# Performance work log

Hardware: AMD Instinct MI355X
Metric: run time of the kernel (lower is better)

## Reference

```python
import jax, jax.numpy as jnp
import numpy as np

N_TP = 4  # number of heterogeneous agent types (experts)


def _mlp(x, w1, b1, w2, b2, w3, b3):
    h = jax.nn.relu(x @ w1 + b1)
    h = jax.nn.relu(h @ w2 + b2)
    return h @ w3 + b3


def setup_inputs() -> dict:
    key = jax.random.key(0)
    ks = jax.random.split(key, 12)
    T, A, D, H, NA = 2048, 128, 64, 64, 16
    s = 0.05
    return {
        "obs": jax.random.normal(ks[0], (T, A, D), dtype=jnp.float32),
        "hete_pick": jax.random.randint(ks[1], (T, A), 0, N_TP, dtype=jnp.int64),
        "gp_sel_summary": jax.random.uniform(ks[2], (T, N_TP), dtype=jnp.float32),
        "W1": jax.random.normal(ks[3], (N_TP, D + N_TP, H), dtype=jnp.float32) * s,
        "b1": jnp.zeros((N_TP, H), jnp.float32),
        "W2": jax.random.normal(ks[4], (N_TP, H, H), dtype=jnp.float32) * s,
        "b2": jnp.zeros((N_TP, H), jnp.float32),
        "W3": jax.random.normal(ks[5], (N_TP, H, NA), dtype=jnp.float32) * s,
        "b3": jnp.zeros((N_TP, NA), jnp.float32),
        "cW1": jax.random.normal(ks[6], (D + N_TP, H), dtype=jnp.float32) * s,
        "cb1": jnp.zeros((H,), jnp.float32),
        "cW2": jax.random.normal(ks[7], (H, H), dtype=jnp.float32) * s,
        "cb2": jnp.zeros((H,), jnp.float32),
        "cW3": jax.random.normal(ks[8], (H, 1), dtype=jnp.float32) * s,
        "cb3": jnp.zeros((1,), jnp.float32),
    }


def reference(obs, hete_pick, gp_sel_summary, W1, b1, W2, b2, W3, b3,
              cW1, cb1, cW2, cb2, cW3, cb3):
    T, A, D = obs.shape
    n_tp = W1.shape[0]
    # hete_info_obs: broadcast group-selection summary over agents, concat to obs
    hete_info = jnp.broadcast_to(gp_sel_summary[:, None, :], (T, A, n_tp))
    x = jnp.concatenate([obs, hete_info.astype(obs.dtype)], axis=-1)  # [T,A,D+n_tp]
    xf = x.reshape(T * A, D + n_tp)
    tp = hete_pick.reshape(T * A)
    # per-type dispatch: mask -> sub-net -> scatter back (expressed as masked select)
    logits = jnp.zeros((T * A, W3.shape[-1]), obs.dtype)
    for t in range(n_tp):
        out_t = _mlp(xf, W1[t], b1[t], W2[t], b2[t], W3[t], b3[t])
        logits = jnp.where((tp == t)[:, None], out_t, logits)
    # central critic runs on all agents
    value = _mlp(xf, cW1, cb1, cW2, cb2, cW3, cb3)  # [T*A,1]
    out = jnp.concatenate([logits, value], axis=-1)  # [T*A, n_action+1]
    return out.reshape(T, A, -1)
```

## Files before the change

### kernel.cpp

```cpp
#include <hip/hip_runtime.h>
#include <stdint.h>


typedef float v4f __attribute__((ext_vector_type(4)));
typedef short v8s __attribute__((ext_vector_type(8)));
typedef short v4s __attribute__((ext_vector_type(4)));
typedef float v4fa __attribute__((ext_vector_type(4), aligned(4)));

#define HS_STR 136
#define WP2_OFF 30720
#define WP3_OFF 51200

#define SEL4(te, a0, a1, a2, a3) \
    ((te) < 2 ? ((te) == 0 ? (a0) : (a1)) : ((te) == 2 ? (a2) : (a3)))

static __device__ __forceinline__ short f2bf(float f) {
    union { __bf16 b; short s; } u;
    u.b = (__bf16)f;
    return u.s;
}

static __device__ __forceinline__ v4s pack4_relu(const v4f a, const v4fa bias) {
    v4s r;
    r[0] = f2bf(fmaxf(a[0] + bias[0], 0.f));
    r[1] = f2bf(fmaxf(a[1] + bias[1], 0.f));
    r[2] = f2bf(fmaxf(a[2] + bias[2], 0.f));
    r[3] = f2bf(fmaxf(a[3] + bias[3], 0.f));
    return r;
}

__global__ void prep_kernel(const float* __restrict__ W1, const float* __restrict__ cW1,
                            const float* __restrict__ W2, const float* __restrict__ cW2,
                            const float* __restrict__ W3, const float* __restrict__ cW3,
                            short* __restrict__ wp) {
    int b = blockIdx.x, lane = threadIdx.x;
    int nl = lane & 15, quad = lane >> 4;
    short frag[8];
    if (b < 60) {
        int e = b / 12, rem = b % 12, ks = rem / 4, nt = rem % 4;
        int n = nt * 16 + nl;
#pragma unroll
        for (int j = 0; j < 8; j++) {
            int k = ks * 32 + quad * 8 + j;
            float v = 0.f;
            if (k < 68) v = (e < 4) ? W1[(e * 68 + k) * 64 + n] : cW1[k * 64 + n];
            frag[j] = f2bf(v);
        }
    } else if (b < 100) {
        int u = b - 60, e = u / 8, ks = (u % 8) / 4, nt = u % 4;
        int n = nt * 16 + nl;
#pragma unroll
        for (int j = 0; j < 8; j++) {
            int k = ks * 32 + quad * 8 + j;
            frag[j] = f2bf((e < 4) ? W2[(e * 64 + k) * 64 + n] : cW2[k * 64 + n]);
        }
    } else {
        int u = b - 100;
#pragma unroll
        for (int j = 0; j < 8; j++) {
            int ks = (u < 8) ? (u & 1) : (u - 8);
            int k  = ks * 32 + quad * 8 + j;
            float v;
            if (u < 8) { int ee = u >> 1; v = W3[(ee * 64 + k) * 16 + nl]; }
            else       { v = (nl == 0) ? cW3[k] : 0.f; }
            frag[j] = f2bf(v);
        }
    }
    v8s pk = { frag[0], frag[1], frag[2], frag[3], frag[4], frag[5], frag[6], frag[7] };
    *(v8s*)(wp + (size_t)b * 512 + lane * 8) = pk;
}


__global__ __launch_bounds__(256, 4) void main_kernel(
    const float* __restrict__ obs, const int* __restrict__ hete,
    const float* __restrict__ gp, const short* __restrict__ wp,
    const float* __restrict__ b1, const float* __restrict__ b2, const float* __restrict__ b3,
    const float* __restrict__ cb1, const float* __restrict__ cb2, const float* __restrict__ cb3,
    float* __restrict__ out)
{
    __shared__ __align__(16) short buf[128 * HS_STR];
    __shared__ int rowtok[128];
    __shared__ int tslot[128];
    __shared__ int wcnt[2][4];

    short* xs = buf;
    short* hs = buf;

    const int b = blockIdx.x;
    const int tid = threadIdx.x, lane = tid & 63, w = tid >> 6;
    const int ml = lane & 15, quad = lane >> 4;
    const size_t base = (size_t)b * 128;

    const int ltk = tid >> 1, hh = tid & 1;
    const float4* src = (const float4*)(obs + (base + ltk) * 64 + hh * 32);
    float4 f[8];
#pragma unroll
    for (int t = 0; t < 8; t++) f[t] = src[t];

    const float* gpb = gp + (size_t)b * 4;
    float g0 = gpb[0], g1 = gpb[1], g2 = gpb[2], g3 = gpb[3];

    int e = 0, rank = 0;
    if (tid < 128) {
        e = hete[base + tid];
        unsigned long long ltm = (1ull << lane) - 1ull;
        unsigned long long m0 = __ballot(e == 0);
        unsigned long long m1 = __ballot(e == 1);
        unsigned long long m2 = __ballot(e == 2);
        unsigned long long m3 = __ballot(e == 3);
        if      (e == 0) rank = __popcll(m0 & ltm);
        else if (e == 1) rank = __popcll(m1 & ltm);
        else if (e == 2) rank = __popcll(m2 & ltm);
        else             rank = __popcll(m3 & ltm);
        if (lane == 0) {
            wcnt[w][0] = __popcll(m0); wcnt[w][1] = __popcll(m1);
            wcnt[w][2] = __popcll(m2); wcnt[w][3] = __popcll(m3);
        }
    }
    __syncthreads();

    const int c0 = wcnt[0][0] + wcnt[1][0];
    const int c1 = wcnt[0][1] + wcnt[1][1];
    const int c2 = wcnt[0][2] + wcnt[1][2];
    const int gs1 = c0, gs2 = c0 + c1, gs3 = c0 + c1 + c2;

    if (tid < 128) {
        int gsE  = SEL4(e, 0, gs1, gs2, gs3);
        int woff = (w == 1) ? wcnt[0][e] : 0;
        int slot = gsE + woff + rank;
        rowtok[slot] = tid;
        tslot[tid]   = slot;
    }
    __syncthreads();

    int teA[8];
#pragma unroll
    for (int mt = 0; mt < 8; mt++)
        teA[mt] = (mt * 16 >= gs1) + (mt * 16 >= gs2) + (mt * 16 >= gs3);

    {
        int s  = tslot[ltk];
        int rb = s * HS_STR + hh * 32;
#pragma unroll
        for (int t = 0; t < 4; t++) {
            float4 a0 = f[2 * t], a1 = f[2 * t + 1];
            v8s pk = { f2bf(a0.x), f2bf(a0.y), f2bf(a0.z), f2bf(a0.w),
                       f2bf(a1.x), f2bf(a1.y), f2bf(a1.z), f2bf(a1.w) };
            *(v8s*)&xs[rb + t * 8] = pk;
        }
        if (hh) {
            v8s pg = { f2bf(g0), f2bf(g1), f2bf(g2), f2bf(g3), 0, 0, 0, 0 };
            v8s z8 = { 0, 0, 0, 0, 0, 0, 0, 0 };
            *(v8s*)&xs[s * HS_STR + 64] = pg;
            *(v8s*)&xs[s * HS_STR + 72] = z8;
            *(v8s*)&xs[s * HS_STR + 80] = z8;
            *(v8s*)&xs[s * HS_STR + 88] = z8;
        }
    }
    __syncthreads();

    v4f accE[8], accC[8];
#pragma unroll
    for (int mt = 0; mt < 8; mt++) { accE[mt] = (v4f){0,0,0,0}; accC[mt] = (v4f){0,0,0,0}; }

    v8s cf1[3];
#pragma unroll
    for (int ks = 0; ks < 3; ks++)
        cf1[ks] = *(const v8s*)(wp + (size_t)((12 + ks) * 4 + w) * 512 + lane * 8);

#pragma unroll
    for (int ks = 0; ks < 3; ks++) {
#pragma unroll
        for (int mt = 0; mt < 8; mt++) {
            v8s aW = *(const v8s*)(wp + (size_t)((teA[mt] * 3 + ks) * 4 + w) * 512 + lane * 8);
            v8s xB = *(const v8s*)&xs[(mt * 16 + ml) * HS_STR + ks * 32 + quad * 8];
            accE[mt] = __builtin_amdgcn_mfma_f32_16x16x32_bf16(aW, xB, accE[mt], 0, 0, 0);
            accC[mt] = __builtin_amdgcn_mfma_f32_16x16x32_bf16(cf1[ks], xB, accC[mt], 0, 0, 0);
        }
    }

    v4f fx[3];
#pragma unroll
    for (int bb = 0; bb < 3; bb++) {
        fx[bb] = (v4f){0,0,0,0};
        int pos = (bb == 0) ? gs1 : (bb == 1) ? gs2 : gs3;
        if (pos & 15) {
            int mtb = pos >> 4, te = bb + 1;
#pragma unroll
            for (int ks = 0; ks < 3; ks++) {
                v8s aW = *(const v8s*)(wp + (size_t)((te * 3 + ks) * 4 + w) * 512 + lane * 8);
                v8s xB = *(const v8s*)&xs[(mtb * 16 + ml) * HS_STR + ks * 32 + quad * 8];
                fx[bb] = __builtin_amdgcn_mfma_f32_16x16x32_bf16(aW, xB, fx[bb], 0, 0, 0);
            }
        }
    }
    __syncthreads();

    {
        v4fa cbv = *(const v4fa*)(cb1 + w * 16 + quad * 4);
#pragma unroll
        for (int mt = 0; mt < 8; mt++) {
            v4fa bv = *(const v4fa*)(b1 + teA[mt] * 64 + w * 16 + quad * 4);
            int rb = (mt * 16 + ml) * HS_STR + w * 16 + quad * 4;
            *(v4s*)&hs[rb]      = pack4_relu(accE[mt], bv);
            *(v4s*)&hs[rb + 64] = pack4_relu(accC[mt], cbv);
        }
#pragma unroll
        for (int bb = 0; bb < 3; bb++) {
            int pos = (bb == 0) ? gs1 : (bb == 1) ? gs2 : gs3;
            if (pos & 15) {
                int mtb = pos >> 4, te = bb + 1;
                int row = mtb * 16 + ml;
                int erow = (row >= gs1) + (row >= gs2) + (row >= gs3);
                if (erow == te) {
                    v4fa bv = *(const v4fa*)(b1 + te * 64 + w * 16 + quad * 4);
                    *(v4s*)&hs[row * HS_STR + w * 16 + quad * 4] = pack4_relu(fx[bb], bv);
                }
            }
        }
    }
    __syncthreads();

    v4f acc2E[8], acc2C[8];
#pragma unroll
    for (int mt = 0; mt < 8; mt++) { acc2E[mt] = (v4f){0,0,0,0}; acc2C[mt] = (v4f){0,0,0,0}; }

    v8s cf2[2];
#pragma unroll
    for (int ks = 0; ks < 2; ks++)
        cf2[ks] = *(const v8s*)(wp + WP2_OFF + (size_t)((8 + ks) * 4 + w) * 512 + lane * 8);

#pragma unroll
    for (int ks = 0; ks < 2; ks++) {
#pragma unroll
        for (int mt = 0; mt < 8; mt++) {
            v8s aW = *(const v8s*)(wp + WP2_OFF + (size_t)((teA[mt] * 2 + ks) * 4 + w) * 512 + lane * 8);
            v8s hE = *(const v8s*)&hs[(mt * 16 + ml) * HS_STR + ks * 32 + quad * 8];
            v8s hC = *(const v8s*)&hs[(mt * 16 + ml) * HS_STR + 64 + ks * 32 + quad * 8];
            acc2E[mt] = __builtin_amdgcn_mfma_f32_16x16x32_bf16(aW, hE, acc2E[mt], 0, 0, 0);
            acc2C[mt] = __builtin_amdgcn_mfma_f32_16x16x32_bf16(cf2[ks], hC, acc2C[mt], 0, 0, 0);
        }
    }

    v4f fx2[3];
#pragma unroll
    for (int bb = 0; bb < 3; bb++) {
        fx2[bb] = (v4f){0,0,0,0};
        int pos = (bb == 0) ? gs1 : (bb == 1) ? gs2 : gs3;
        if (pos & 15) {
            int mtb = pos >> 4, te = bb + 1;
#pragma unroll
            for (int ks = 0; ks < 2; ks++) {
                v8s aW = *(const v8s*)(wp + WP2_OFF + (size_t)((te * 2 + ks) * 4 + w) * 512 + lane * 8);
                v8s hE = *(const v8s*)&hs[(mtb * 16 + ml) * HS_STR + ks * 32 + quad * 8];
                fx2[bb] = __builtin_amdgcn_mfma_f32_16x16x32_bf16(aW, hE, fx2[bb], 0, 0, 0);
            }
        }
    }
    __syncthreads();

    {
        v4fa cbv = *(const v4fa*)(cb2 + w * 16 + quad * 4);
#pragma unroll
        for (int mt = 0; mt < 8; mt++) {
            v4fa bv = *(const v4fa*)(b2 + teA[mt] * 64 + w * 16 + quad * 4);
            int rb = (mt * 16 + ml) * HS_STR + w * 16 + quad * 4;
            *(v4s*)&hs[rb]      = pack4_relu(acc2E[mt], bv);
            *(v4s*)&hs[rb + 64] = pack4_relu(acc2C[mt], cbv);
        }
#pragma unroll
        for (int bb = 0; bb < 3; bb++) {
            int pos = (bb == 0) ? gs1 : (bb == 1) ? gs2 : gs3;
            if (pos & 15) {
                int mtb = pos >> 4, te = bb + 1;
                int row = mtb * 16 + ml;
                int erow = (row >= gs1) + (row >= gs2) + (row >= gs3);
                if (erow == te) {
                    v4fa bv = *(const v4fa*)(b2 + te * 64 + w * 16 + quad * 4);
                    *(v4s*)&hs[row * HS_STR + w * 16 + quad * 4] = pack4_relu(fx2[bb], bv);
                }
            }
        }
    }
    __syncthreads();

    v4f accL[2], accV[2];
#pragma unroll
    for (int j = 0; j < 2; j++) { accL[j] = (v4f){0,0,0,0}; accV[j] = (v4f){0,0,0,0}; }

#pragma unroll
    for (int ks = 0; ks < 2; ks++) {
        v8s aV = *(const v8s*)(wp + WP3_OFF + (size_t)(8 + ks) * 512 + lane * 8);
#pragma unroll
        for (int j = 0; j < 2; j++) {
            int mt = w + 4 * j;
            int te = (mt * 16 >= gs1) + (mt * 16 >= gs2) + (mt * 16 >= gs3);
            v8s aW = *(const v8s*)(wp + WP3_OFF + (size_t)(te * 2 + ks) * 512 + lane * 8);
            v8s hE = *(const v8s*)&hs[(mt * 16 + ml) * HS_STR + ks * 32 + quad * 8];
            v8s hC = *(const v8s*)&hs[(mt * 16 + ml) * HS_STR + 64 + ks * 32 + quad * 8];
            accL[j] = __builtin_amdgcn_mfma_f32_16x16x32_bf16(aW, hE, accL[j], 0, 0, 0);
            accV[j] = __builtin_amdgcn_mfma_f32_16x16x32_bf16(aV, hC, accV[j], 0, 0, 0);
        }
    }

    v4f fxL[3];
#pragma unroll
    for (int bb = 0; bb < 3; bb++) {
        fxL[bb] = (v4f){0,0,0,0};
        int pos = (bb == 0) ? gs1 : (bb == 1) ? gs2 : gs3;
        int mtb = pos >> 4;
        if ((pos & 15) && (mtb & 3) == w) {
            int te = bb + 1;
#pragma unroll
            for (int ks = 0; ks < 2; ks++) {
                v8s aW = *(const v8s*)(wp + WP3_OFF + (size_t)(te * 2 + ks) * 512 + lane * 8);
                v8s hE = *(const v8s*)&hs[(mtb * 16 + ml) * HS_STR + ks * 32 + quad * 8];
                fxL[bb] = __builtin_amdgcn_mfma_f32_16x16x32_bf16(aW, hE, fxL[bb], 0, 0, 0);
            }
        }
    }

    {
        float cb3v = cb3[0];
#pragma unroll
        for (int j = 0; j < 2; j++) {
            int mt = w + 4 * j;
            int te = (mt * 16 >= gs1) + (mt * 16 >= gs2) + (mt * 16 >= gs3);
            int row = mt * 16 + ml;
            int erow = (row >= gs1) + (row >= gs2) + (row >= gs3);
            int tk = rowtok[row];
            float* o = out + (base + (size_t)tk) * 17;
            if (erow == te) {
                v4fa b3v = *(const v4fa*)(b3 + te * 16 + quad * 4);
                v4fa ov = { accL[j][0] + b3v[0], accL[j][1] + b3v[1],
                            accL[j][2] + b3v[2], accL[j][3] + b3v[3] };
                *(v4fa*)(o + quad * 4) = ov;
            }
            if (quad == 0) o[16] = accV[j][0] + cb3v;
        }
#pragma unroll
        for (int bb = 0; bb < 3; bb++) {
            int pos = (bb == 0) ? gs1 : (bb == 1) ? gs2 : gs3;
            int mtb = pos >> 4;
            if ((pos & 15) && (mtb & 3) == w) {
                int row = mtb * 16 + ml;
                int erow = (row >= gs1) + (row >= gs2) + (row >= gs3);
                if (erow == bb + 1) {
                    v4fa b3v = *(const v4fa*)(b3 + (bb + 1) * 16 + quad * 4);
                    int tk = rowtok[row];
                    float* o = out + (base + (size_t)tk) * 17;
                    v4fa ov = { fxL[bb][0] + b3v[0], fxL[bb][1] + b3v[1],
                                fxL[bb][2] + b3v[2], fxL[bb][3] + b3v[3] };
                    *(v4fa*)(o + quad * 4) = ov;
                }
            }
        }
    }
}


extern "C" void kernel_launch(void* const* d_in, const int* in_sizes, int n_in,
                              void* d_out, int out_size, void* d_ws, size_t ws_size,
                              hipStream_t stream) {
    const float* obs = (const float*)d_in[0];
    const int*  hete = (const int*)d_in[1];
    const float* gp  = (const float*)d_in[2];
    const float* W1  = (const float*)d_in[3];
    const float* b1  = (const float*)d_in[4];
    const float* W2  = (const float*)d_in[5];
    const float* b2  = (const float*)d_in[6];
    const float* W3  = (const float*)d_in[7];
    const float* b3  = (const float*)d_in[8];
    const float* cW1 = (const float*)d_in[9];
    const float* cb1 = (const float*)d_in[10];
    const float* cW2 = (const float*)d_in[11];
    const float* cb2 = (const float*)d_in[12];
    const float* cW3 = (const float*)d_in[13];
    const float* cb3 = (const float*)d_in[14];
    float* out = (float*)d_out;

    short* wp = (short*)d_ws;

    prep_kernel<<<110,  64, 0, stream>>>(W1, cW1, W2, cW2, W3, cW3, wp);
    main_kernel<<<2048, 256, 0, stream>>>(obs, hete, gp, wp,
                                          b1, b2, b3, cb1, cb2, cb3, out);
}
```

Measured before the change: 158.1 us.

## Fold per-timestep gp term and biases into MFMA accumulator init, skip third K-step

Measured after the change: 159.4 us. No clear change (+0.8%).

```diff
diff --git a/kernel.cpp b/kernel.cpp
--- a/kernel.cpp
+++ b/kernel.cpp
@@ -7,9 +7,11 @@
 typedef short v4s __attribute__((ext_vector_type(4)));
 typedef float v4fa __attribute__((ext_vector_type(4), aligned(4)));
 
+#define XS_STR 72
 #define HS_STR 136
-#define WP2_OFF 30720
-#define WP3_OFF 51200
+#define WP2_OFF  30720
+#define WP3_OFF  51200
+#define WPB2_OFF 56320
 
 #define SEL4(te, a0, a1, a2, a3) \
     ((te) < 2 ? ((te) == 0 ? (a0) : (a1)) : ((te) == 2 ? (a2) : (a3)))
@@ -20,18 +22,20 @@
     return u.s;
 }
 
-static __device__ __forceinline__ v4s pack4_relu(const v4f a, const v4fa bias) {
+static __device__ __forceinline__ v4s pack4r(const v4f a) {
     v4s r;
-    r[0] = f2bf(fmaxf(a[0] + bias[0], 0.f));
-    r[1] = f2bf(fmaxf(a[1] + bias[1], 0.f));
-    r[2] = f2bf(fmaxf(a[2] + bias[2], 0.f));
-    r[3] = f2bf(fmaxf(a[3] + bias[3], 0.f));
+    r[0] = f2bf(fmaxf(a[0], 0.f));
+    r[1] = f2bf(fmaxf(a[1], 0.f));
+    r[2] = f2bf(fmaxf(a[2], 0.f));
+    r[3] = f2bf(fmaxf(a[3], 0.f));
     return r;
 }
 
 __global__ void prep_kernel(const float* __restrict__ W1, const float* __restrict__ cW1,
                             const float* __restrict__ W2, const float* __restrict__ cW2,
                             const float* __restrict__ W3, const float* __restrict__ cW3,
+                            const float* __restrict__ b1, const float* __restrict__ cb1,
+                            const float* __restrict__ b2, const float* __restrict__ cb2,
                             short* __restrict__ wp) {
     int b = blockIdx.x, lane = threadIdx.x;
     int nl = lane & 15, quad = lane >> 4;
@@ -43,7 +47,8 @@
         for (int j = 0; j < 8; j++) {
             int k = ks * 32 + quad * 8 + j;
             float v = 0.f;
-            if (k < 68) v = (e < 4) ? W1[(e * 68 + k) * 64 + n] : cW1[k * 64 + n];
+            if (k < 68)       v = (e < 4) ? W1[(e * 68 + k) * 64 + n] : cW1[k * 64 + n];
+            else if (k == 68) v = (e < 4) ? b1[e * 64 + n] : cb1[n];
             frag[j] = f2bf(v);
         }
     } else if (b < 100) {
@@ -54,7 +59,7 @@
             int k = ks * 32 + quad * 8 + j;
             frag[j] = f2bf((e < 4) ? W2[(e * 64 + k) * 64 + n] : cW2[k * 64 + n]);
         }
-    } else {
+    } else if (b < 110) {
         int u = b - 100;
 #pragma unroll
         for (int j = 0; j < 8; j++) {
@@ -65,6 +70,15 @@
             else       { v = (nl == 0) ? cW3[k] : 0.f; }
             frag[j] = f2bf(v);
         }
+    } else {
+        int u = b - 110, net = u / 4, nt = u % 4;
+        int n = nt * 16 + nl;
+#pragma unroll
+        for (int j = 0; j < 8; j++) {
+            float v = 0.f;
+            if (quad == 0 && j == 0) v = (net < 4) ? b2[net * 64 + n] : cb2[n];
+            frag[j] = f2bf(v);
+        }
     }
     v8s pk = { frag[0], frag[1], frag[2], frag[3], frag[4], frag[5], frag[6], frag[7] };
     *(v8s*)(wp + (size_t)b * 512 + lane * 8) = pk;
@@ -74,8 +88,7 @@
 __global__ __launch_bounds__(256, 4) void main_kernel(
     const float* __restrict__ obs, const int* __restrict__ hete,
     const float* __restrict__ gp, const short* __restrict__ wp,
-    const float* __restrict__ b1, const float* __restrict__ b2, const float* __restrict__ b3,
-    const float* __restrict__ cb1, const float* __restrict__ cb2, const float* __restrict__ cb3,
+    const float* __restrict__ b3, const float* __restrict__ cb3,
     float* __restrict__ out)
 {
     __shared__ __align__(16) short buf[128 * HS_STR];
@@ -122,10 +135,13 @@
     const int c0 = wcnt[0][0] + wcnt[1][0];
     const int c1 = wcnt[0][1] + wcnt[1][1];
     const int c2 = wcnt[0][2] + wcnt[1][2];
-    const int gs1 = c0, gs2 = c0 + c1, gs3 = c0 + c1 + c2;
+    const int sgs1 = __builtin_amdgcn_readfirstlane(c0);
+    const int sgs2 = __builtin_amdgcn_readfirstlane(c0 + c1);
+    const int sgs3 = __builtin_amdgcn_readfirstlane(c0 + c1 + c2);
+    const int SG[5] = { 0, sgs1, sgs2, sgs3, 128 };
 
     if (tid < 128) {
-        int gsE  = SEL4(e, 0, gs1, gs2, gs3);
+        int gsE  = SEL4(e, 0, sgs1, sgs2, sgs3);
         int woff = (w == 1) ? wcnt[0][e] : 0;
         int slot = gsE + woff + rank;
         rowtok[slot] = tid;
@@ -133,14 +149,9 @@
     }
     __syncthreads();
 
-    int teA[8];
-#pragma unroll
-    for (int mt = 0; mt < 8; mt++)
-        teA[mt] = (mt * 16 >= gs1) + (mt * 16 >= gs2) + (mt * 16 >= gs3);
-
     {
         int s  = tslot[ltk];
-        int rb = s * HS_STR + hh * 32;
+        int rb = s * XS_STR + hh * 32;
 #pragma unroll
         for (int t = 0; t < 4; t++) {
             float4 a0 = f[2 * t], a1 = f[2 * t + 1];
@@ -148,82 +159,118 @@
                        f2bf(a1.x), f2bf(a1.y), f2bf(a1.z), f2bf(a1.w) };
             *(v8s*)&xs[rb + t * 8] = pk;
         }
-        if (hh) {
-            v8s pg = { f2bf(g0), f2bf(g1), f2bf(g2), f2bf(g3), 0, 0, 0, 0 };
-            v8s z8 = { 0, 0, 0, 0, 0, 0, 0, 0 };
-            *(v8s*)&xs[s * HS_STR + 64] = pg;
-            *(v8s*)&xs[s * HS_STR + 72] = z8;
-            *(v8s*)&xs[s * HS_STR + 80] = z8;
-            *(v8s*)&xs[s * HS_STR + 88] = z8;
-        }
-    }
-    __syncthreads();
-
-    v4f accE[8], accC[8];
-#pragma unroll
-    for (int mt = 0; mt < 8; mt++) { accE[mt] = (v4f){0,0,0,0}; accC[mt] = (v4f){0,0,0,0}; }
-
-    v8s cf1[3];
-#pragma unroll
-    for (int ks = 0; ks < 3; ks++)
+    }
+
+    v8s gfrag = (v8s){0,0,0,0,0,0,0,0};
+    v8s onef  = (v8s){0,0,0,0,0,0,0,0};
+    if (quad == 0) {
+        gfrag[0] = f2bf(g0); gfrag[1] = f2bf(g1);
+        gfrag[2] = f2bf(g2); gfrag[3] = f2bf(g3);
+        gfrag[4] = (short)0x3F80;
+        onef[0]  = (short)0x3F80;
+    }
+    __syncthreads();
+
+    v4f accE[8], accC[8], fx[3];
+#pragma unroll
+    for (int mt = 0; mt < 8; mt++) { accE[mt] = (v4f){0,0,0,0}; }
+    fx[0] = fx[1] = fx[2] = (v4f){0,0,0,0};
+
+    {
+        v8s cW2 = *(const v8s*)(wp + (size_t)(14 * 4 + w) * 512 + lane * 8);
+        v4f tC = __builtin_amdgcn_mfma_f32_16x16x32_bf16(cW2, gfrag, (v4f){0,0,0,0}, 0, 0, 0);
+#pragma unroll
+        for (int mt = 0; mt < 8; mt++) accC[mt] = tC;
+    }
+#pragma unroll
+    for (int te = 0; te < 4; te++) {
+        int lo = SG[te], hi = SG[te + 1];
+        if (lo < hi) {
+            v8s aW2 = *(const v8s*)(wp + (size_t)((te * 3 + 2) * 4 + w) * 512 + lane * 8);
+            v4f tE = __builtin_amdgcn_mfma_f32_16x16x32_bf16(aW2, gfrag, (v4f){0,0,0,0}, 0, 0, 0);
+#pragma unroll
+            for (int mt = 0; mt < 8; mt++)
+                if (mt * 16 >= lo && mt * 16 < hi) accE[mt] = tE;
+            if (te > 0 && (lo & 15)) fx[te - 1] = tE;
+        }
+    }
+
+    v8s cf1[2];
+#pragma unroll
+    for (int ks = 0; ks < 2; ks++)
         cf1[ks] = *(const v8s*)(wp + (size_t)((12 + ks) * 4 + w) * 512 + lane * 8);
 
 #pragma unroll
-    for (int ks = 0; ks < 3; ks++) {
+    for (int ks = 0; ks < 2; ks++) {
 #pragma unroll
         for (int mt = 0; mt < 8; mt++) {
-            v8s aW = *(const v8s*)(wp + (size_t)((teA[mt] * 3 + ks) * 4 + w) * 512 + lane * 8);
-            v8s xB = *(const v8s*)&xs[(mt * 16 + ml) * HS_STR + ks * 32 + quad * 8];
-            accE[mt] = __builtin_amdgcn_mfma_f32_16x16x32_bf16(aW, xB, accE[mt], 0, 0, 0);
-            accC[mt] = __builtin_amdgcn_mfma_f32_16x16x32_bf16(cf1[ks], xB, accC[mt], 0, 0, 0);
-        }
-    }
-
-    v4f fx[3];
-#pragma unroll
-    for (int bb = 0; bb < 3; bb++) {
-        fx[bb] = (v4f){0,0,0,0};
-        int pos = (bb == 0) ? gs1 : (bb == 1) ? gs2 : gs3;
-        if (pos & 15) {
-            int mtb = pos >> 4, te = bb + 1;
-#pragma unroll
-            for (int ks = 0; ks < 3; ks++) {
+            v8s xb = *(const v8s*)&xs[(mt * 16 + ml) * XS_STR + ks * 32 + quad * 8];
+            accC[mt] = __builtin_amdgcn_mfma_f32_16x16x32_bf16(cf1[ks], xb, accC[mt], 0, 0, 0);
+        }
+#pragma unroll
+        for (int te = 0; te < 4; te++) {
+            int lo = SG[te], hi = SG[te + 1];
+            if (lo < hi) {
                 v8s aW = *(const v8s*)(wp + (size_t)((te * 3 + ks) * 4 + w) * 512 + lane * 8);
-                v8s xB = *(const v8s*)&xs[(mtb * 16 + ml) * HS_STR + ks * 32 + quad * 8];
-                fx[bb] = __builtin_amdgcn_mfma_f32_16x16x32_bf16(aW, xB, fx[bb], 0, 0, 0);
-            }
-        }
-    }
-    __syncthreads();
-
-    {
-        v4fa cbv = *(const v4fa*)(cb1 + w * 16 + quad * 4);
+#pragma unroll
+                for (int mt = 0; mt < 8; mt++) {
+                    if (mt * 16 >= lo && mt * 16 < hi) {
+                        v8s xb = *(const v8s*)&xs[(mt * 16 + ml) * XS_STR + ks * 32 + quad * 8];
+                        accE[mt] = __builtin_amdgcn_mfma_f32_16x16x32_bf16(aW, xb, accE[mt], 0, 0, 0);
+                    }
+                    if (te > 0 && (lo & 15) && (lo >> 4) == mt) {
+                        v8s xb = *(const v8s*)&xs[(mt * 16 + ml) * XS_STR + ks * 32 + quad * 8];
+                        fx[te - 1] = __builtin_amdgcn_mfma_f32_16x16x32_bf16(aW, xb, fx[te - 1], 0, 0, 0);
+                    }
+                }
+            }
+        }
+    }
+    __syncthreads();
+
+    {
 #pragma unroll
         for (int mt = 0; mt < 8; mt++) {
-            v4fa bv = *(const v4fa*)(b1 + teA[mt] * 64 + w * 16 + quad * 4);
             int rb = (mt * 16 + ml) * HS_STR + w * 16 + quad * 4;
-            *(v4s*)&hs[rb]      = pack4_relu(accE[mt], bv);
-            *(v4s*)&hs[rb + 64] = pack4_relu(accC[mt], cbv);
+            *(v4s*)&hs[rb]      = pack4r(accE[mt]);
+            *(v4s*)&hs[rb + 64] = pack4r(accC[mt]);
         }
 #pragma unroll
         for (int bb = 0; bb < 3; bb++) {
-            int pos = (bb == 0) ? gs1 : (bb == 1) ? gs2 : gs3;
-            if (pos & 15) {
-                int mtb = pos >> 4, te = bb + 1;
-                int row = mtb * 16 + ml;
-                int erow = (row >= gs1) + (row >= gs2) + (row >= gs3);
-                if (erow == te) {
-                    v4fa bv = *(const v4fa*)(b1 + te * 64 + w * 16 + quad * 4);
-                    *(v4s*)&hs[row * HS_STR + w * 16 + quad * 4] = pack4_relu(fx[bb], bv);
-                }
-            }
-        }
-    }
-    __syncthreads();
-
-    v4f acc2E[8], acc2C[8];
-#pragma unroll
-    for (int mt = 0; mt < 8; mt++) { acc2E[mt] = (v4f){0,0,0,0}; acc2C[mt] = (v4f){0,0,0,0}; }
+            int lo = SG[bb + 1], hi = SG[bb + 2];
+            if ((lo & 15) && lo < hi) {
+                int row  = (lo >> 4) * 16 + ml;
+                int erow = (row >= sgs1) + (row >= sgs2) + (row >= sgs3);
+                if (erow == bb + 1)
+                    *(v4s*)&hs[row * HS_STR + w * 16 + quad * 4] = pack4r(fx[bb]);
+            }
+        }
+    }
+    __syncthreads();
+
+    v4f acc2E[8], acc2C[8], fx2[3];
+#pragma unroll
+    for (int mt = 0; mt < 8; mt++) { acc2E[mt] = (v4f){0,0,0,0}; }
+    fx2[0] = fx2[1] = fx2[2] = (v4f){0,0,0,0};
+
+    {
+        v8s cbf = *(const v8s*)(wp + WPB2_OFF + (size_t)(16 + w) * 512 + lane * 8);
+        v4f tC = __builtin_amdgcn_mfma_f32_16x16x32_bf16(cbf, onef, (v4f){0,0,0,0}, 0, 0, 0);
+#pragma unroll
+        for (int mt = 0; mt < 8; mt++) acc2C[mt] = tC;
+    }
+#pragma unroll
+    for (int te = 0; te < 4; te++) {
+        int lo = SG[te], hi = SG[te + 1];
+        if (lo < hi) {
+            v8s bf = *(const v8s*)(wp + WPB2_OFF + (size_t)(te * 4 + w) * 512 + lane * 8);
+            v4f tE = __builtin_amdgcn_mfma_f32_16x16x32_bf16(bf, onef, (v4f){0,0,0,0}, 0, 0, 0);
+#pragma unroll
+            for (int mt = 0; mt < 8; mt++)
+                if (mt * 16 >= lo && mt * 16 < hi) acc2E[mt] = tE;
+            if (te > 0 && (lo & 15)) fx2[te - 1] = tE;
+        }
+    }
 
     v8s cf2[2];
 #pragma unroll
@@ -234,51 +281,45 @@
     for (int ks = 0; ks < 2; ks++) {
 #pragma unroll
         for (int mt = 0; mt < 8; mt++) {
-            v8s aW = *(const v8s*)(wp + WP2_OFF + (size_t)((teA[mt] * 2 + ks) * 4 + w) * 512 + lane * 8);
-            v8s hE = *(const v8s*)&hs[(mt * 16 + ml) * HS_STR + ks * 32 + quad * 8];
             v8s hC = *(const v8s*)&hs[(mt * 16 + ml) * HS_STR + 64 + ks * 32 + quad * 8];
-            acc2E[mt] = __builtin_amdgcn_mfma_f32_16x16x32_bf16(aW, hE, acc2E[mt], 0, 0, 0);
             acc2C[mt] = __builtin_amdgcn_mfma_f32_16x16x32_bf16(cf2[ks], hC, acc2C[mt], 0, 0, 0);
         }
-    }
-
-    v4f fx2[3];
-#pragma unroll
-    for (int bb = 0; bb < 3; bb++) {
-        fx2[bb] = (v4f){0,0,0,0};
-        int pos = (bb == 0) ? gs1 : (bb == 1) ? gs2 : gs3;
-        if (pos & 15) {
-            int mtb = pos >> 4, te = bb + 1;
-#pragma unroll
-            for (int ks = 0; ks < 2; ks++) {
+#pragma unroll
+        for (int te = 0; te < 4; te++) {
+            int lo = SG[te], hi = SG[te + 1];
+            if (lo < hi) {
                 v8s aW = *(const v8s*)(wp + WP2_OFF + (size_t)((te * 2 + ks) * 4 + w) * 512 + lane * 8);
-                v8s hE = *(const v8s*)&hs[(mtb * 16 + ml) * HS_STR + ks * 32 + quad * 8];
-                fx2[bb] = __builtin_amdgcn_mfma_f32_16x16x32_bf16(aW, hE, fx2[bb], 0, 0, 0);
-            }
-        }
-    }
-    __syncthreads();
-
-    {
-        v4fa cbv = *(const v4fa*)(cb2 + w * 16 + quad * 4);
+#pragma unroll
+                for (int mt = 0; mt < 8; mt++) {
+                    if (mt * 16 >= lo && mt * 16 < hi) {
+                        v8s hE = *(const v8s*)&hs[(mt * 16 + ml) * HS_STR + ks * 32 + quad * 8];
+                        acc2E[mt] = __builtin_amdgcn_mfma_f32_16x16x32_bf16(aW, hE, acc2E[mt], 0, 0, 0);
+                    }
+                    if (te > 0 && (lo & 15) && (lo >> 4) == mt) {
+                        v8s hE = *(const v8s*)&hs[(mt * 16 + ml) * HS_STR + ks * 32 + quad * 8];
+                        fx2[te - 1] = __builtin_amdgcn_mfma_f32_16x16x32_bf16(aW, hE, fx2[te - 1], 0, 0, 0);
+                    }
+                }
+            }
+        }
+    }
+    __syncthreads();
+
+    {
 #pragma unroll
         for (int mt = 0; mt < 8; mt++) {
-            v4fa bv = *(const v4fa*)(b2 + teA[mt] * 64 + w * 16 + quad * 4);
             int rb = (mt * 16 + ml) * HS_STR + w * 16 + quad * 4;
-            *(v4s*)&hs[rb]      = pack4_relu(acc2E[mt], bv);
-            *(v4s*)&hs[rb + 64] = pack4_relu(acc2C[mt], cbv);
+            *(v4s*)&hs[rb]      = pack4r(acc2E[mt]);
+            *(v4s*)&hs[rb + 64] = pack4r(acc2C[mt]);
         }
 #pragma unroll
         for (int bb = 0; bb < 3; bb++) {
-            int pos = (bb == 0) ? gs1 : (bb == 1) ? gs2 : gs3;
-            if (pos & 15) {
-                int mtb = pos >> 4, te = bb + 1;
-                int row = mtb * 16 + ml;
-                int erow = (row >= gs1) + (row >= gs2) + (row >= gs3);
-                if (erow == te) {
-                    v4fa bv = *(const v4fa*)(b2 + te * 64 + w * 16 + quad * 4);
-                    *(v4s*)&hs[row * HS_STR + w * 16 + quad * 4] = pack4_relu(fx2[bb], bv);
-                }
+            int lo = SG[bb + 1], hi = SG[bb + 2];
+            if ((lo & 15) && lo < hi) {
+                int row  = (lo >> 4) * 16 + ml;
+                int erow = (row >= sgs1) + (row >= sgs2) + (row >= sgs3);
+                if (erow == bb + 1)
+                    *(v4s*)&hs[row * HS_STR + w * 16 + quad * 4] = pack4r(fx2[bb]);
             }
         }
     }
@@ -294,7 +335,7 @@
 #pragma unroll
         for (int j = 0; j < 2; j++) {
             int mt = w + 4 * j;
-            int te = (mt * 16 >= gs1) + (mt * 16 >= gs2) + (mt * 16 >= gs3);
+            int te = (mt * 16 >= sgs1) + (mt * 16 >= sgs2) + (mt * 16 >= sgs3);
             v8s aW = *(const v8s*)(wp + WP3_OFF + (size_t)(te * 2 + ks) * 512 + lane * 8);
             v8s hE = *(const v8s*)&hs[(mt * 16 + ml) * HS_STR + ks * 32 + quad * 8];
             v8s hC = *(const v8s*)&hs[(mt * 16 + ml) * HS_STR + 64 + ks * 32 + quad * 8];
@@ -307,13 +348,12 @@
 #pragma unroll
     for (int bb = 0; bb < 3; bb++) {
         fxL[bb] = (v4f){0,0,0,0};
-        int pos = (bb == 0) ? gs1 : (bb == 1) ? gs2 : gs3;
-        int mtb = pos >> 4;
-        if ((pos & 15) && (mtb & 3) == w) {
-            int te = bb + 1;
+        int lo = SG[bb + 1], hi = SG[bb + 2];
+        int mtb = lo >> 4;
+        if ((lo & 15) && lo < hi && (mtb & 3) == w) {
 #pragma unroll
             for (int ks = 0; ks < 2; ks++) {
-                v8s aW = *(const v8s*)(wp + WP3_OFF + (size_t)(te * 2 + ks) * 512 + lane * 8);
+                v8s aW = *(const v8s*)(wp + WP3_OFF + (size_t)((bb + 1) * 2 + ks) * 512 + lane * 8);
                 v8s hE = *(const v8s*)&hs[(mtb * 16 + ml) * HS_STR + ks * 32 + quad * 8];
                 fxL[bb] = __builtin_amdgcn_mfma_f32_16x16x32_bf16(aW, hE, fxL[bb], 0, 0, 0);
             }
@@ -325,9 +365,9 @@
 #pragma unroll
         for (int j = 0; j < 2; j++) {
             int mt = w + 4 * j;
-            int te = (mt * 16 >= gs1) + (mt * 16 >= gs2) + (mt * 16 >= gs3);
+            int te = (mt * 16 >= sgs1) + (mt * 16 >= sgs2) + (mt * 16 >= sgs3);
             int row = mt * 16 + ml;
-            int erow = (row >= gs1) + (row >= gs2) + (row >= gs3);
+            int erow = (row >= sgs1) + (row >= sgs2) + (row >= sgs3);
             int tk = rowtok[row];
             float* o = out + (base + (size_t)tk) * 17;
             if (erow == te) {
@@ -340,11 +380,11 @@
         }
 #pragma unroll
         for (int bb = 0; bb < 3; bb++) {
-            int pos = (bb == 0) ? gs1 : (bb == 1) ? gs2 : gs3;
-            int mtb = pos >> 4;
-            if ((pos & 15) && (mtb & 3) == w) {
+            int lo = SG[bb + 1], hi = SG[bb + 2];
+            int mtb = lo >> 4;
+            if ((lo & 15) && lo < hi && (mtb & 3) == w) {
                 int row = mtb * 16 + ml;
-                int erow = (row >= gs1) + (row >= gs2) + (row >= gs3);
+                int erow = (row >= sgs1) + (row >= sgs2) + (row >= sgs3);
                 if (erow == bb + 1) {
                     v4fa b3v = *(const v4fa*)(b3 + (bb + 1) * 16 + quad * 4);
                     int tk = rowtok[row];
@@ -381,7 +421,7 @@
 
     short* wp = (short*)d_ws;
 
-    prep_kernel<<<110,  64, 0, stream>>>(W1, cW1, W2, cW2, W3, cW3, wp);
-    main_kernel<<<2048, 256, 0, stream>>>(obs, hete, gp, wp,
-                                          b1, b2, b3, cb1, cb2, cb3, out);
+    prep_kernel<<<130,  64, 0, stream>>>(W1, cW1, W2, cW2, W3, cW3,
+                                         b1, cb1, b2, cb2, wp);
+    main_kernel<<<2048, 256, 0, stream>>>(obs, hete, gp, wp, b3, cb3, out);
 }
```
